# Optimization experiments

Measured on AMD Instinct MI355X. Metric: run time of the kernel, lower is better.

The kernel has to match this reference:

```python
import jax, jax.numpy as jnp
import numpy as np


def setup_inputs() -> dict:
    key = jax.random.key(0)
    B, S, K = 4, 4096, 64
    attn_scores = jax.random.normal(key, (B, S, S), dtype=jnp.float32)
    return {"attn_scores": attn_scores, "k": K}


def reference(attn_scores, k):
    # attn_scores: [B, S, S]; k: python int
    B, S, _ = attn_scores.shape
    # topk over last dim -> indices [B, S, k]
    _, idx = jax.lax.top_k(attn_scores, k)
    # torch.scatter(newmask, 1, idx, zeros): newmask[b, idx[b,s,j], j] = False
    # for s in range(S), j in range(k) (only first k columns are written).
    mask = jnp.ones((B, S, S), dtype=bool)
    b = jnp.arange(B)[:, None, None]      # [B,1,1]
    j = jnp.arange(k)[None, None, :]      # [1,1,k]
    mask = mask.at[b, idx, j].set(False)  # scatter False along row dim
    # triangular overwrite: for i in range(k+1): mask[:, i, i+1:] = True
    rows = jnp.arange(S)[:, None]         # [S,1]
    cols = jnp.arange(S)[None, :]         # [1,S]
    tri = (rows < (k + 1)) & (cols > rows)  # [S,S]
    mask = jnp.where(tri[None, :, :], True, mask)
    return mask[:, None, :, :]            # [B,1,S,S]
```

## Files before the change

### kernel.cpp

```cpp
#include <hip/hip_runtime.h>
#include <stdint.h>

#define S_DIM 4096
#define K_TOP 64
#define THREADS 256
#define EPT 16
#define CAND_MAX 256

__global__ __launch_bounds__(256) void fill_ones_kernel(int4* __restrict__ out, int n4) {
    int i = blockIdx.x * blockDim.x + threadIdx.x;
    const int stride = gridDim.x * blockDim.x;
    const int4 v = make_int4(1, 1, 1, 1);
    for (; i < n4; i += stride) out[i] = v;
}

__global__ __launch_bounds__(256) void topk_scatter_kernel(const float* __restrict__ scores,
                                                           int* __restrict__ out) {
    const int row = blockIdx.x;
    const int b   = row >> 12;
    const int t   = threadIdx.x;

    __shared__ uint32_t hist[256];
    __shared__ uint32_t sfx[256];
    __shared__ unsigned long long cand[CAND_MAX];
    __shared__ uint32_t sh_prefix, sh_remaining, sh_count;

    const float4* rowp = (const float4*)(scores + (size_t)row * S_DIM);
    uint32_t key[EPT];
    #pragma unroll
    for (int i = 0; i < 4; ++i) {
        float4 v = rowp[i * THREADS + t];
        float f[4] = {v.x, v.y, v.z, v.w};
        #pragma unroll
        for (int c = 0; c < 4; ++c) {
            uint32_t ub = __float_as_uint(f[c]);
            key[i * 4 + c] = (ub & 0x80000000u) ? ~ub : (ub | 0x80000000u);
        }
    }

    if (t == 0) { sh_count = 0u; }

    uint32_t prefix = 0u;
    uint32_t remaining = K_TOP;

    #pragma unroll
    for (int pass = 0; pass < 4; ++pass) {
        const int shift = 24 - pass * 8;
        hist[t] = 0u;
        __syncthreads();

        #pragma unroll
        for (int i = 0; i < EPT; ++i) {
            uint32_t kk = key[i];
            bool active;
            if (pass == 0) active = true;
            else           active = ((kk ^ prefix) >> (shift + 8)) == 0u;
            if (active) atomicAdd(&hist[(kk >> shift) & 0xFFu], 1u);
        }
        __syncthreads();

        uint32_t* src = hist;
        uint32_t* dst = sfx;
        #pragma unroll
        for (int off = 1; off < 256; off <<= 1) {
            uint32_t v = src[t];
            if (t + off < 256) v += src[t + off];
            dst[t] = v;
            __syncthreads();
            uint32_t* tmp = src; src = dst; dst = tmp;
        }
        uint32_t ge = src[t];
        uint32_t gt = (t == 255) ? 0u : src[t + 1];
        if (ge >= remaining && gt < remaining) {
            sh_prefix    = prefix | ((uint32_t)t << shift);
            sh_remaining = remaining - gt;
        }
        __syncthreads();
        prefix    = sh_prefix;
        remaining = sh_remaining;
    }

    const uint32_t T = prefix;

    #pragma unroll
    for (int i = 0; i < EPT; ++i) {
        if (key[i] >= T) {
            uint32_t idx = (((uint32_t)(i >> 2) * THREADS + (uint32_t)t) << 2) | (uint32_t)(i & 3);
            uint32_t pos = atomicAdd(&sh_count, 1u);
            if (pos < CAND_MAX) {
                cand[pos] = ((unsigned long long)key[i] << 32) | (uint32_t)(~idx);
            }
        }
    }
    __syncthreads();

    uint32_t m = sh_count;
    if (m > CAND_MAX) m = CAND_MAX;

    if ((uint32_t)t < m) {
        unsigned long long me = cand[t];
        uint32_t rank = 0;
        for (uint32_t i = 0; i < m; ++i) rank += (cand[i] > me) ? 1u : 0u;
        if (rank < K_TOP) {
            uint32_t idx = ~(uint32_t)me;
            if (idx >= rank) {
                out[(size_t)b * ((size_t)S_DIM * S_DIM) + (size_t)idx * S_DIM + rank] = 0;
            }
        }
    }
}

extern "C" void kernel_launch(void* const* d_in, const int* in_sizes, int n_in,
                              void* d_out, int out_size, void* d_ws, size_t ws_size,
                              hipStream_t stream) {
    const float* scores = (const float*)d_in[0];
    int* out = (int*)d_out;

    const int n4 = out_size / 4;
    hipLaunchKernelGGL(fill_ones_kernel, dim3(2048), dim3(THREADS), 0, stream,
                       (int4*)out, n4);

    const int B = in_sizes[0] / (S_DIM * S_DIM);
    hipLaunchKernelGGL(topk_scatter_kernel, dim3(B * S_DIM), dim3(THREADS), 0, stream,
                       scores, out);
}
```

Measured before the change: 510.8 us.

## Replace radix-select threshold with wave bitonic sort of per-thread maxima

Replaces the four-pass shared-memory radix histogram select with a cheaper threshold: each thread takes the max of its 16 keys, each 64-lane wave bitonic-sorts those maxima with shuffles and takes its 16th largest, and the block threshold is the minimum over the four waves. This removes many atomics and syncthreads-heavy scans. The candidate set must then be ranked by brute force, and a slow 64-round argmax fallback handles the case where more than 256 candidates pass the threshold.

After: 455.9 us. -10.8%, faster.

```diff
diff --git a/kernel.cpp b/kernel.cpp
--- a/kernel.cpp
+++ b/kernel.cpp
@@ -5,7 +5,7 @@
 #define K_TOP 64
 #define THREADS 256
 #define EPT 16
-#define CAND_MAX 256
+#define CAND_CAP 256
 
 __global__ __launch_bounds__(256) void fill_ones_kernel(int4* __restrict__ out, int n4) {
     int i = blockIdx.x * blockDim.x + threadIdx.x;
@@ -14,16 +14,26 @@
     for (; i < n4; i += stride) out[i] = v;
 }
 
+__device__ __forceinline__ unsigned long long shfl_xor_u64(unsigned long long v, int m) {
+    uint32_t lo = (uint32_t)v, hi = (uint32_t)(v >> 32);
+    lo = __shfl_xor(lo, m, 64);
+    hi = __shfl_xor(hi, m, 64);
+    return ((unsigned long long)hi << 32) | lo;
+}
+
 __global__ __launch_bounds__(256) void topk_scatter_kernel(const float* __restrict__ scores,
                                                            int* __restrict__ out) {
-    const int row = blockIdx.x;
-    const int b   = row >> 12;
-    const int t   = threadIdx.x;
+    const int row  = blockIdx.x;
+    const int b    = row >> 12;
+    const int t    = threadIdx.x;
+    const int lane = t & 63;
+    const int wid  = t >> 6;
 
-    __shared__ uint32_t hist[256];
-    __shared__ uint32_t sfx[256];
-    __shared__ unsigned long long cand[CAND_MAX];
-    __shared__ uint32_t sh_prefix, sh_remaining, sh_count;
+    __shared__ uint32_t sh_w16[4];
+    __shared__ unsigned long long cand[CAND_CAP];
+    __shared__ uint32_t sh_count;
+    __shared__ unsigned long long sh_wbest[4];
+    __shared__ unsigned long long sh_best;
 
     const float4* rowp = (const float4*)(scores + (size_t)row * S_DIM);
     uint32_t key[EPT];
@@ -38,75 +48,94 @@
         }
     }
 
-    if (t == 0) { sh_count = 0u; }
+    if (t == 0) sh_count = 0u;
 
-    uint32_t prefix = 0u;
-    uint32_t remaining = K_TOP;
+    uint32_t mx = key[0];
+    #pragma unroll
+    for (int i = 1; i < EPT; ++i) mx = max(mx, key[i]);
 
+    uint32_t x = mx;
     #pragma unroll
-    for (int pass = 0; pass < 4; ++pass) {
-        const int shift = 24 - pass * 8;
-        hist[t] = 0u;
-        __syncthreads();
+    for (int k = 2; k <= 64; k <<= 1) {
+        #pragma unroll
+        for (int j = k >> 1; j > 0; j >>= 1) {
+            uint32_t v = __shfl_xor(x, j, 64);
+            bool keepMin = (((lane & j) == 0) == ((lane & k) == 0));
+            x = keepMin ? min(x, v) : max(x, v);
+        }
+    }
+    uint32_t w16 = __shfl(x, 48, 64);
+    if (lane == 0) sh_w16[wid] = w16;
+    __syncthreads();
 
-        #pragma unroll
-        for (int i = 0; i < EPT; ++i) {
-            uint32_t kk = key[i];
-            bool active;
-            if (pass == 0) active = true;
-            else           active = ((kk ^ prefix) >> (shift + 8)) == 0u;
-            if (active) atomicAdd(&hist[(kk >> shift) & 0xFFu], 1u);
-        }
-        __syncthreads();
-
-        uint32_t* src = hist;
-        uint32_t* dst = sfx;
-        #pragma unroll
-        for (int off = 1; off < 256; off <<= 1) {
-            uint32_t v = src[t];
-            if (t + off < 256) v += src[t + off];
-            dst[t] = v;
-            __syncthreads();
-            uint32_t* tmp = src; src = dst; dst = tmp;
-        }
-        uint32_t ge = src[t];
-        uint32_t gt = (t == 255) ? 0u : src[t + 1];
-        if (ge >= remaining && gt < remaining) {
-            sh_prefix    = prefix | ((uint32_t)t << shift);
-            sh_remaining = remaining - gt;
-        }
-        __syncthreads();
-        prefix    = sh_prefix;
-        remaining = sh_remaining;
-    }
-
-    const uint32_t T = prefix;
+    const uint32_t Tc = min(min(sh_w16[0], sh_w16[1]), min(sh_w16[2], sh_w16[3]));
 
     #pragma unroll
     for (int i = 0; i < EPT; ++i) {
-        if (key[i] >= T) {
+        if (key[i] >= Tc) {
             uint32_t idx = (((uint32_t)(i >> 2) * THREADS + (uint32_t)t) << 2) | (uint32_t)(i & 3);
             uint32_t pos = atomicAdd(&sh_count, 1u);
-            if (pos < CAND_MAX) {
+            if (pos < CAND_CAP) {
                 cand[pos] = ((unsigned long long)key[i] << 32) | (uint32_t)(~idx);
             }
         }
     }
     __syncthreads();
+    const uint32_t m = sh_count;
 
-    uint32_t m = sh_count;
-    if (m > CAND_MAX) m = CAND_MAX;
-
-    if ((uint32_t)t < m) {
-        unsigned long long me = cand[t];
-        uint32_t rank = 0;
-        for (uint32_t i = 0; i < m; ++i) rank += (cand[i] > me) ? 1u : 0u;
-        if (rank < K_TOP) {
-            uint32_t idx = ~(uint32_t)me;
-            if (idx >= rank) {
-                out[(size_t)b * ((size_t)S_DIM * S_DIM) + (size_t)idx * S_DIM + rank] = 0;
+    if (m <= CAND_CAP) {
+        if ((uint32_t)t < m) {
+            unsigned long long me = cand[t];
+            uint32_t rank = 0;
+            for (uint32_t i = 0; i < m; ++i) rank += (cand[i] > me) ? 1u : 0u;
+            if (rank < K_TOP) {
+                uint32_t idx = ~(uint32_t)me;
+                if (idx >= rank) {
+                    out[(size_t)b * ((size_t)S_DIM * S_DIM) + (size_t)idx * S_DIM + rank] = 0;
+                }
             }
         }
+        return;
+    }
+
+    uint32_t used = 0u;
+    for (int r = 0; r < K_TOP; ++r) {
+        unsigned long long best = 0ull;
+        #pragma unroll
+        for (int i = 0; i < EPT; ++i) {
+            if (!(used & (1u << i))) {
+                uint32_t idx = (((uint32_t)(i >> 2) * THREADS + (uint32_t)t) << 2) | (uint32_t)(i & 3);
+                unsigned long long ck = ((unsigned long long)key[i] << 32) | (uint32_t)(~idx);
+                if (ck > best) best = ck;
+            }
+        }
+        #pragma unroll
+        for (int off = 32; off > 0; off >>= 1) {
+            unsigned long long o = shfl_xor_u64(best, off);
+            if (o > best) best = o;
+        }
+        if (lane == 0) sh_wbest[wid] = best;
+        __syncthreads();
+        if (t == 0) {
+            unsigned long long bb = sh_wbest[0];
+            for (int w = 1; w < 4; ++w) if (sh_wbest[w] > bb) bb = sh_wbest[w];
+            sh_best = bb;
+        }
+        __syncthreads();
+        const unsigned long long gb = sh_best;
+        #pragma unroll
+        for (int i = 0; i < EPT; ++i) {
+            uint32_t idx = (((uint32_t)(i >> 2) * THREADS + (uint32_t)t) << 2) | (uint32_t)(i & 3);
+            unsigned long long ck = ((unsigned long long)key[i] << 32) | (uint32_t)(~idx);
+            if (ck == gb) {
+                used |= (1u << i);
+                uint32_t oidx = ~(uint32_t)gb;
+                if (oidx >= (uint32_t)r) {
+                    out[(size_t)b * ((size_t)S_DIM * S_DIM) + (size_t)oidx * S_DIM + r] = 0;
+                }
+            }
+        }
+        __syncthreads();
     }
 }
 
```
